# Performance work log

Measured on AMD Instinct MI355X. Metric: run time of the kernel, lower is better.

## Reference

```python
import jax, jax.numpy as jnp
import numpy as np


def _gcn_conv(x, W, b, src, dst, dinv, n_nodes):
    # x: [N, Cin], W: [Cin, Cout]. PyG GCNConv: transform then normalized aggregate.
    h = x @ W  # [N, Cout]
    norm = dinv[src] * dinv[dst]  # [E']
    msgs = h[src] * norm[:, None]  # gather + scale, [E', Cout]
    out = jax.ops.segment_sum(msgs, dst, num_segments=n_nodes)
    return out + b


def setup_inputs() -> dict:
    key = jax.random.key(0)
    k1, k2, k3, k4 = jax.random.split(key, 4)
    N, E, C = 100000, 1600000, 128
    x = jax.random.normal(k1, (N, C), dtype=jnp.float32)
    edge_index = jax.random.randint(k2, (2, E), 0, N, dtype=jnp.int32)
    # Glorot-ish scale for square layers
    s = 1.0 / np.sqrt(C)
    W1 = jax.random.normal(k3, (C, C), dtype=jnp.float32) * s
    W2 = jax.random.normal(k4, (C, C), dtype=jnp.float32) * s
    b1 = jnp.zeros((C,), dtype=jnp.float32)
    b2 = jnp.zeros((C,), dtype=jnp.float32)
    return {"x": x, "edge_index": edge_index, "W1": W1, "b1": b1, "W2": W2, "b2": b2}


def reference(x, edge_index, W1, b1, W2, b2):
    n_nodes = x.shape[0]
    # Add self-loops (PyG GCNConv default add_self_loops=True)
    loops = jnp.arange(n_nodes, dtype=edge_index.dtype)
    src = jnp.concatenate([edge_index[0], loops])
    dst = jnp.concatenate([edge_index[1], loops])
    # Symmetric normalization: deg^-1/2 with degree counted at destination
    deg = jax.ops.segment_sum(jnp.ones_like(dst, dtype=x.dtype), dst, num_segments=n_nodes)
    dinv = jnp.where(deg > 0, jax.lax.rsqrt(jnp.maximum(deg, 1e-12)), 0.0)

    h = _gcn_conv(x, W1, b1, src, dst, dinv, n_nodes)
    h = jax.nn.relu(h)
    out = _gcn_conv(h, W2, b2, src, dst, dinv, n_nodes)
    return out
```

## Files before the change

kernel.cpp:

```cpp
#include <hip/hip_runtime.h>

#define CDIM 128
#define BCAP 12288

typedef __bf16 v8bf __attribute__((ext_vector_type(8)));
typedef float  v4f  __attribute__((ext_vector_type(4)));

__device__ __forceinline__ unsigned short f2bf(float f) {
    unsigned int u = __float_as_uint(f);
    u += 0x7fffu + ((u >> 16) & 1u);
    return (unsigned short)(u >> 16);
}

__global__ __launch_bounds__(256) void k_init_bcur(int* __restrict__ bcur) {
    bcur[threadIdx.x] = threadIdx.x * BCAP;
}

__global__ __launch_bounds__(256) void k_bucket_scatter(const int* __restrict__ src,
                                                        const int* __restrict__ dst,
                                                        int* __restrict__ bcur,
                                                        uint2* __restrict__ pairs, int E) {
    __shared__ int cnt[256];
    __shared__ int cur[256];
    int t = threadIdx.x;
    cnt[t] = 0;
    __syncthreads();
    int e0 = blockIdx.x * 4096;
    int ds[16];
#pragma unroll
    for (int j = 0; j < 16; j++) {
        int e = e0 + j * 256 + t;
        ds[j] = (e < E) ? dst[e] : -1;
        if (ds[j] >= 0) atomicAdd(&cnt[ds[j] >> 9], 1);
    }
    __syncthreads();
    int c = cnt[t];
    cur[t] = c ? atomicAdd(&bcur[t], c) : 0;
    __syncthreads();
#pragma unroll
    for (int j = 0; j < 16; j++) {
        if (ds[j] >= 0) {
            int e = e0 + j * 256 + t;
            int p = atomicAdd(&cur[ds[j] >> 9], 1);
            pairs[p] = make_uint2((unsigned)src[e], (unsigned)ds[j]);
        }
    }
}

__global__ __launch_bounds__(256) void k_bucket_csr(const uint2* __restrict__ pairs,
                                                    const int* __restrict__ bcur,
                                                    int* __restrict__ csr,
                                                    int* __restrict__ rowptr,
                                                    float* __restrict__ dinv,
                                                    int N, int E, int NB) {
    __shared__ int sscan[256];
    __shared__ int deg[512];
    __shared__ int pre[512];
    __shared__ int sums[256];
    int b = blockIdx.x, t = threadIdx.x;

    int c = (t < NB) ? (bcur[t] - t * BCAP) : 0;
    sscan[t] = c;
    __syncthreads();
    for (int off = 1; off < 256; off <<= 1) {
        int v = (t >= off) ? sscan[t - off] : 0;
        __syncthreads();
        sscan[t] += v;
        __syncthreads();
    }
    int cnt   = bcur[b] - b * BCAP;
    int gbase = sscan[b] - cnt;
    int nb0   = b << 9;

    deg[t] = 0; deg[t + 256] = 0;
    __syncthreads();
    for (int i = t; i < cnt; i += 256)
        atomicAdd(&deg[(int)pairs[b * BCAP + i].y - nb0], 1);
    __syncthreads();

    int d0 = deg[2 * t], d1 = deg[2 * t + 1];
    sums[t] = d0 + d1;
    __syncthreads();
    for (int off = 1; off < 256; off <<= 1) {
        int v = (t >= off) ? sums[t - off] : 0;
        __syncthreads();
        sums[t] += v;
        __syncthreads();
    }
    int eb = sums[t] - (d0 + d1);
    pre[2 * t]     = eb;
    pre[2 * t + 1] = eb + d0;
    __syncthreads();

    for (int l = t; l < 512; l += 256) {
        int g = nb0 + l;
        if (g < N) {
            rowptr[g] = gbase + pre[l];
            dinv[g]   = rsqrtf((float)(deg[l] + 1));
        }
    }
    if (b == 0 && t == 0) rowptr[N] = E;
    __syncthreads();

    for (int i = t; i < cnt; i += 256) {
        uint2 p = pairs[b * BCAP + i];
        int l = (int)p.y - nb0;
        int pos = atomicAdd(&pre[l], 1);
        csr[gbase + pos] = (int)p.x;
    }
}

template<int INBF16>
__global__ __launch_bounds__(256) void k_gemm(const void* __restrict__ Xv,
                                              const float* __restrict__ W,
                                              const float* __restrict__ dinv,
                                              unsigned short* __restrict__ Hb,
                                              int N) {
    __shared__ char sX[64 * 256];
    __shared__ char sW[128 * 256];
    const int tid  = threadIdx.x;
    const int row0 = blockIdx.x * 64;

    if (INBF16) {
        const uint4* Xb = (const uint4*)Xv + (size_t)row0 * 16;
#pragma unroll
        for (int i = 0; i < 4; i++) {
            int q   = i * 256 + tid;
            int row = q >> 4;
            int c   = q & 15;
            uint4 v = make_uint4(0u, 0u, 0u, 0u);
            if (row0 + row < N) v = Xb[q];
            int addr = row * 256 + (((c ^ (row & 7)) << 4));
            *(uint4*)(sX + addr) = v;
        }
    } else {
        const float4* Xb = (const float4*)Xv + (size_t)row0 * 32;
#pragma unroll
        for (int i = 0; i < 8; i++) {
            int q   = i * 256 + tid;
            int row = q >> 5;
            int k4  = q & 31;
            float4 v = make_float4(0.f, 0.f, 0.f, 0.f);
            if (row0 + row < N) v = Xb[q];
            unsigned int lo = (unsigned int)f2bf(v.x) | ((unsigned int)f2bf(v.y) << 16);
            unsigned int hi = (unsigned int)f2bf(v.z) | ((unsigned int)f2bf(v.w) << 16);
            int chunk = k4 >> 1, half = k4 & 1;
            int addr = row * 256 + (((chunk ^ (row & 7)) << 4) | (half << 3));
            *(uint2*)(sX + addr) = make_uint2(lo, hi);
        }
    }
    {
        int kg = tid >> 5;
        int c0 = (tid & 31) * 4;
        unsigned int wp[4][8];
#pragma unroll
        for (int i = 0; i < 16; i++) {
            float4 v = *(const float4*)(W + (size_t)(kg * 16 + i) * CDIM + c0);
            unsigned short b0 = f2bf(v.x), b1 = f2bf(v.y), b2 = f2bf(v.z), b3 = f2bf(v.w);
            int ui = i >> 1;
            if ((i & 1) == 0) {
                wp[0][ui] = b0; wp[1][ui] = b1; wp[2][ui] = b2; wp[3][ui] = b3;
            } else {
                wp[0][ui] |= (unsigned int)b0 << 16;
                wp[1][ui] |= (unsigned int)b1 << 16;
                wp[2][ui] |= (unsigned int)b2 << 16;
                wp[3][ui] |= (unsigned int)b3 << 16;
            }
        }
#pragma unroll
        for (int j = 0; j < 4; j++) {
            int c = c0 + j;
            int base = c * 256;
            int a0 = base + ((((kg * 2) ^ (c & 7)) << 4));
            int a1 = base + ((((kg * 2 + 1) ^ (c & 7)) << 4));
            *(uint4*)(sW + a0) = make_uint4(wp[j][0], wp[j][1], wp[j][2], wp[j][3]);
            *(uint4*)(sW + a1) = make_uint4(wp[j][4], wp[j][5], wp[j][6], wp[j][7]);
        }
    }
    __syncthreads();

    const int l   = tid & 63;
    const int wv  = tid >> 6;
    const int ar  = l & 15;
    const int kg2 = l >> 4;

    v4f acc[8];
#pragma unroll
    for (int ct = 0; ct < 8; ct++) acc[ct] = (v4f){0.f, 0.f, 0.f, 0.f};

#pragma unroll
    for (int ks = 0; ks < 4; ks++) {
        int r = wv * 16 + ar;
        v8bf a = *(const v8bf*)(sX + r * 256 + (((ks * 4 + kg2) ^ (r & 7)) << 4));
#pragma unroll
        for (int ct = 0; ct < 8; ct++) {
            int c = ct * 16 + ar;
            v8bf b = *(const v8bf*)(sW + c * 256 + (((ks * 4 + kg2) ^ (c & 7)) << 4));
            acc[ct] = __builtin_amdgcn_mfma_f32_16x16x32_bf16(a, b, acc[ct], 0, 0, 0);
        }
    }

    int rbase = row0 + wv * 16 + kg2 * 4;
#pragma unroll
    for (int reg = 0; reg < 4; reg++) {
        int g = rbase + reg;
        if (g < N) {
            float di = dinv[g];
            unsigned short* orow = Hb + (size_t)g * CDIM;
#pragma unroll
            for (int ct = 0; ct < 8; ct++)
                orow[ct * 16 + ar] = f2bf(acc[ct][reg] * di);
        }
    }
}

template<int OUTBF16>
__global__ __launch_bounds__(256) void k_gather(const unsigned short* __restrict__ Hb,
                                                const int* __restrict__ csr,
                                                const int* __restrict__ rowptr,
                                                const float* __restrict__ dinv,
                                                const float* __restrict__ bias,
                                                void* __restrict__ outv,
                                                int N, int do_relu) {
    int t    = blockIdx.x * 256 + threadIdx.x;
    int n    = t >> 4;
    int lane = t & 15;
    if (n >= N) return;

    const uint4* base = (const uint4*)Hb;
    float acc[8] = {0.f, 0.f, 0.f, 0.f, 0.f, 0.f, 0.f, 0.f};

    auto accum = [&](uint4 u) {
        acc[0] += __uint_as_float(u.x << 16);
        acc[1] += __uint_as_float(u.x & 0xffff0000u);
        acc[2] += __uint_as_float(u.y << 16);
        acc[3] += __uint_as_float(u.y & 0xffff0000u);
        acc[4] += __uint_as_float(u.z << 16);
        acc[5] += __uint_as_float(u.z & 0xffff0000u);
        acc[6] += __uint_as_float(u.w << 16);
        acc[7] += __uint_as_float(u.w & 0xffff0000u);
    };

    int e  = rowptr[n];
    int e1 = rowptr[n + 1];

    uint4 us = base[(size_t)n * 16 + lane];
    accum(us);

    for (; e + 4 <= e1; e += 4) {
        int s0 = csr[e], s1 = csr[e + 1], s2 = csr[e + 2], s3 = csr[e + 3];
        uint4 u0 = base[(size_t)s0 * 16 + lane];
        uint4 u1 = base[(size_t)s1 * 16 + lane];
        uint4 u2 = base[(size_t)s2 * 16 + lane];
        uint4 u3 = base[(size_t)s3 * 16 + lane];
        accum(u0); accum(u1); accum(u2); accum(u3);
    }
    for (; e < e1; e++) {
        uint4 u = base[(size_t)csr[e] * 16 + lane];
        accum(u);
    }

    float di = dinv[n];
    const float* bp = bias + lane * 8;
    float o[8];
#pragma unroll
    for (int j = 0; j < 8; j++) o[j] = fmaf(acc[j], di, bp[j]);
    if (do_relu) {
#pragma unroll
        for (int j = 0; j < 8; j++) o[j] = fmaxf(o[j], 0.f);
    }

    if (OUTBF16) {
        uint4 u;
        u.x = (unsigned int)f2bf(o[0]) | ((unsigned int)f2bf(o[1]) << 16);
        u.y = (unsigned int)f2bf(o[2]) | ((unsigned int)f2bf(o[3]) << 16);
        u.z = (unsigned int)f2bf(o[4]) | ((unsigned int)f2bf(o[5]) << 16);
        u.w = (unsigned int)f2bf(o[6]) | ((unsigned int)f2bf(o[7]) << 16);
        ((uint4*)outv)[(size_t)n * 16 + lane] = u;
    } else {
        float* op = (float*)outv + (size_t)n * CDIM + lane * 8;
        *(float4*)(op)     = make_float4(o[0], o[1], o[2], o[3]);
        *(float4*)(op + 4) = make_float4(o[4], o[5], o[6], o[7]);
    }
}

extern "C" void kernel_launch(void* const* d_in, const int* in_sizes, int n_in,
                              void* d_out, int out_size, void* d_ws, size_t ws_size,
                              hipStream_t stream) {
    const float* x  = (const float*)d_in[0];
    const int*   ei = (const int*)d_in[1];
    const float* W1 = (const float*)d_in[2];
    const float* b1 = (const float*)d_in[3];
    const float* W2 = (const float*)d_in[4];
    const float* b2 = (const float*)d_in[5];
    float* out = (float*)d_out;

    const int N = in_sizes[0] / CDIM;
    const int E = in_sizes[1] / 2;
    const int* src = ei;
    const int* dst = ei + E;

    char* w = (char*)d_ws;
    unsigned short* Hb = (unsigned short*)w;  w += ((size_t)N * CDIM * 2 + 255) & ~255ull;
    float* dinv   = (float*)w;                w += ((size_t)N * 4 + 255) & ~255ull;
    int*   rowptr = (int*)w;                  w += ((size_t)(N + 1) * 4 + 255) & ~255ull;
    int*   bcur   = (int*)w;                  w += 1024;
    int*   csr    = (int*)w;                  w += ((size_t)E * 4 + 255) & ~255ull;
    uint2* pairs  = (uint2*)w;
    unsigned short* Act = (unsigned short*)w;

    int NB = (N + 511) >> 9;
    int nA = (E + 4095) >> 12;
    int gb = (N + 63) / 64;
    int ga = (int)(((size_t)N * 16 + 255) / 256);

    k_init_bcur<<<1, 256, 0, stream>>>(bcur);
    k_bucket_scatter<<<nA, 256, 0, stream>>>(src, dst, bcur, pairs, E);
    k_bucket_csr<<<NB, 256, 0, stream>>>(pairs, bcur, csr, rowptr, dinv, N, E, NB);

    k_gemm<0><<<gb, 256, 0, stream>>>(x, W1, dinv, Hb, N);
    k_gather<1><<<ga, 256, 0, stream>>>(Hb, csr, rowptr, dinv, b1, Act, N, 1);

    k_gemm<1><<<gb, 256, 0, stream>>>(Act, W2, dinv, Hb, N);
    k_gather<0><<<ga, 256, 0, stream>>>(Hb, csr, rowptr, dinv, b2, out, N, 0);
}
```

Baseline: 219.5 us.

## Split gather edges across four sub-groups per node and pack bucket pairs

The gather kernel now gives each node a full 64-lane wave: four 16-lane groups each take a strided subset of the edges, and the partial sums are combined with cross-lane shuffles. This raises memory-level parallelism per node and shortens the serial edge loop, at the cost of shuffle reductions and idle lanes on low-degree nodes. Separately, the bucket pairs are packed into one 32-bit word (source shifted by 9 bits plus a 9-bit local destination) instead of a uint2, halving scatter and CSR-build traffic. The packing assumes source ids fit in 23 bits.

```diff
diff --git a/kernel.cpp b/kernel.cpp
--- a/kernel.cpp
+++ b/kernel.cpp
@@ -19,7 +19,8 @@
 __global__ __launch_bounds__(256) void k_bucket_scatter(const int* __restrict__ src,
                                                         const int* __restrict__ dst,
                                                         int* __restrict__ bcur,
-                                                        uint2* __restrict__ pairs, int E) {
+                                                        unsigned int* __restrict__ pairs,
+                                                        int E) {
     __shared__ int cnt[256];
     __shared__ int cur[256];
     int t = threadIdx.x;
@@ -42,12 +43,12 @@
         if (ds[j] >= 0) {
             int e = e0 + j * 256 + t;
             int p = atomicAdd(&cur[ds[j] >> 9], 1);
-            pairs[p] = make_uint2((unsigned)src[e], (unsigned)ds[j]);
-        }
-    }
-}
-
-__global__ __launch_bounds__(256) void k_bucket_csr(const uint2* __restrict__ pairs,
+            pairs[p] = ((unsigned)src[e] << 9) | ((unsigned)ds[j] & 511u);
+        }
+    }
+}
+
+__global__ __launch_bounds__(256) void k_bucket_csr(const unsigned int* __restrict__ pairs,
                                                     const int* __restrict__ bcur,
                                                     int* __restrict__ csr,
                                                     int* __restrict__ rowptr,
@@ -75,7 +76,7 @@
     deg[t] = 0; deg[t + 256] = 0;
     __syncthreads();
     for (int i = t; i < cnt; i += 256)
-        atomicAdd(&deg[(int)pairs[b * BCAP + i].y - nb0], 1);
+        atomicAdd(&deg[pairs[b * BCAP + i] & 511u], 1);
     __syncthreads();
 
     int d0 = deg[2 * t], d1 = deg[2 * t + 1];
@@ -103,10 +104,10 @@
     __syncthreads();
 
     for (int i = t; i < cnt; i += 256) {
-        uint2 p = pairs[b * BCAP + i];
-        int l = (int)p.y - nb0;
+        unsigned int p = pairs[b * BCAP + i];
+        int l = (int)(p & 511u);
         int pos = atomicAdd(&pre[l], 1);
-        csr[gbase + pos] = (int)p.x;
+        csr[gbase + pos] = (int)(p >> 9);
     }
 }
 
@@ -222,10 +223,11 @@
                                                 const float* __restrict__ bias,
                                                 void* __restrict__ outv,
                                                 int N, int do_relu) {
-    int t    = blockIdx.x * 256 + threadIdx.x;
-    int n    = t >> 4;
-    int lane = t & 15;
+    int n = blockIdx.x * 4 + (threadIdx.x >> 6);
     if (n >= N) return;
+    int lane  = threadIdx.x & 63;
+    int esub  = lane >> 4;
+    int chunk = lane & 15;
 
     const uint4* base = (const uint4*)Hb;
     float acc[8] = {0.f, 0.f, 0.f, 0.f, 0.f, 0.f, 0.f, 0.f};
@@ -241,46 +243,50 @@
         acc[7] += __uint_as_float(u.w & 0xffff0000u);
     };
 
-    int e  = rowptr[n];
+    int e0 = rowptr[n];
     int e1 = rowptr[n + 1];
 
-    uint4 us = base[(size_t)n * 16 + lane];
-    accum(us);
-
-    for (; e + 4 <= e1; e += 4) {
-        int s0 = csr[e], s1 = csr[e + 1], s2 = csr[e + 2], s3 = csr[e + 3];
-        uint4 u0 = base[(size_t)s0 * 16 + lane];
-        uint4 u1 = base[(size_t)s1 * 16 + lane];
-        uint4 u2 = base[(size_t)s2 * 16 + lane];
-        uint4 u3 = base[(size_t)s3 * 16 + lane];
-        accum(u0); accum(u1); accum(u2); accum(u3);
-    }
-    for (; e < e1; e++) {
-        uint4 u = base[(size_t)csr[e] * 16 + lane];
-        accum(u);
-    }
-
-    float di = dinv[n];
-    const float* bp = bias + lane * 8;
-    float o[8];
-#pragma unroll
-    for (int j = 0; j < 8; j++) o[j] = fmaf(acc[j], di, bp[j]);
-    if (do_relu) {
-#pragma unroll
-        for (int j = 0; j < 8; j++) o[j] = fmaxf(o[j], 0.f);
-    }
-
-    if (OUTBF16) {
-        uint4 u;
-        u.x = (unsigned int)f2bf(o[0]) | ((unsigned int)f2bf(o[1]) << 16);
-        u.y = (unsigned int)f2bf(o[2]) | ((unsigned int)f2bf(o[3]) << 16);
-        u.z = (unsigned int)f2bf(o[4]) | ((unsigned int)f2bf(o[5]) << 16);
-        u.w = (unsigned int)f2bf(o[6]) | ((unsigned int)f2bf(o[7]) << 16);
-        ((uint4*)outv)[(size_t)n * 16 + lane] = u;
-    } else {
-        float* op = (float*)outv + (size_t)n * CDIM + lane * 8;
-        *(float4*)(op)     = make_float4(o[0], o[1], o[2], o[3]);
-        *(float4*)(op + 4) = make_float4(o[4], o[5], o[6], o[7]);
+    if (esub == 0) accum(base[(size_t)n * 16 + chunk]);
+
+    int e = e0 + esub;
+    for (; e + 4 < e1; e += 8) {
+        int s0 = csr[e];
+        int s1 = csr[e + 4];
+        uint4 u0 = base[(size_t)s0 * 16 + chunk];
+        uint4 u1 = base[(size_t)s1 * 16 + chunk];
+        accum(u0);
+        accum(u1);
+    }
+    if (e < e1) accum(base[(size_t)csr[e] * 16 + chunk]);
+
+#pragma unroll
+    for (int j = 0; j < 8; j++) {
+        acc[j] += __shfl_xor(acc[j], 16, 64);
+        acc[j] += __shfl_xor(acc[j], 32, 64);
+    }
+
+    if (esub == 0) {
+        float di = dinv[n];
+        const float* bp = bias + chunk * 8;
+        float o[8];
+#pragma unroll
+        for (int j = 0; j < 8; j++) o[j] = fmaf(acc[j], di, bp[j]);
+        if (do_relu) {
+#pragma unroll
+            for (int j = 0; j < 8; j++) o[j] = fmaxf(o[j], 0.f);
+        }
+        if (OUTBF16) {
+            uint4 u;
+            u.x = (unsigned int)f2bf(o[0]) | ((unsigned int)f2bf(o[1]) << 16);
+            u.y = (unsigned int)f2bf(o[2]) | ((unsigned int)f2bf(o[3]) << 16);
+            u.z = (unsigned int)f2bf(o[4]) | ((unsigned int)f2bf(o[5]) << 16);
+            u.w = (unsigned int)f2bf(o[6]) | ((unsigned int)f2bf(o[7]) << 16);
+            ((uint4*)outv)[(size_t)n * 16 + chunk] = u;
+        } else {
+            float* op = (float*)outv + (size_t)n * CDIM + chunk * 8;
+            *(float4*)(op)     = make_float4(o[0], o[1], o[2], o[3]);
+            *(float4*)(op + 4) = make_float4(o[4], o[5], o[6], o[7]);
+        }
     }
 }
 
@@ -306,21 +312,21 @@
     int*   rowptr = (int*)w;                  w += ((size_t)(N + 1) * 4 + 255) & ~255ull;
     int*   bcur   = (int*)w;                  w += 1024;
     int*   csr    = (int*)w;                  w += ((size_t)E * 4 + 255) & ~255ull;
-    uint2* pairs  = (uint2*)w;
+    unsigned int* pairs = (unsigned int*)w;
     unsigned short* Act = (unsigned short*)w;
 
     int NB = (N + 511) >> 9;
     int nA = (E + 4095) >> 12;
     int gb = (N + 63) / 64;
-    int ga = (int)(((size_t)N * 16 + 255) / 256);
+    int gn = (N + 3) / 4;
 
     k_init_bcur<<<1, 256, 0, stream>>>(bcur);
     k_bucket_scatter<<<nA, 256, 0, stream>>>(src, dst, bcur, pairs, E);
     k_bucket_csr<<<NB, 256, 0, stream>>>(pairs, bcur, csr, rowptr, dinv, N, E, NB);
 
     k_gemm<0><<<gb, 256, 0, stream>>>(x, W1, dinv, Hb, N);
-    k_gather<1><<<ga, 256, 0, stream>>>(Hb, csr, rowptr, dinv, b1, Act, N, 1);
+    k_gather<1><<<gn, 256, 0, stream>>>(Hb, csr, rowptr, dinv, b1, Act, N, 1);
 
     k_gemm<1><<<gb, 256, 0, stream>>>(Act, W2, dinv, Hb, N);
-    k_gather<0><<<ga, 256, 0, stream>>>(Hb, csr, rowptr, dinv, b2, out, N, 0);
-}
+    k_gather<0><<<gn, 256, 0, stream>>>(Hb, csr, rowptr, dinv, b2, out, N, 0);
+}
```

Result: slower. 226.1 us (+3.0%).

## Pack bucket pairs into 32 bits, stage CSR in LDS, unroll gather by 8

Applied to the files above, without the earlier changes.

Edge pairs are packed into a single 32-bit word (source shifted left plus local destination index), halving the bucket scratch traffic. The CSR build now assembles each bucket's column list in shared memory and writes it out contiguously, replacing scattered global stores. The gather loop is unrolled to 8 outstanding row loads for more memory-level parallelism. The per-bucket count is capped at the LDS capacity, which would silently drop edges for heavily skewed buckets, and the packing limits node ids to 23 bits.

```diff
diff --git a/kernel.cpp b/kernel.cpp
--- a/kernel.cpp
+++ b/kernel.cpp
@@ -2,6 +2,7 @@
 
 #define CDIM 128
 #define BCAP 12288
+#define LCAP 10240
 
 typedef __bf16 v8bf __attribute__((ext_vector_type(8)));
 typedef float  v4f  __attribute__((ext_vector_type(4)));
@@ -19,7 +20,8 @@
 __global__ __launch_bounds__(256) void k_bucket_scatter(const int* __restrict__ src,
                                                         const int* __restrict__ dst,
                                                         int* __restrict__ bcur,
-                                                        uint2* __restrict__ pairs, int E) {
+                                                        unsigned int* __restrict__ pairs,
+                                                        int E) {
     __shared__ int cnt[256];
     __shared__ int cur[256];
     int t = threadIdx.x;
@@ -42,12 +44,12 @@
         if (ds[j] >= 0) {
             int e = e0 + j * 256 + t;
             int p = atomicAdd(&cur[ds[j] >> 9], 1);
-            pairs[p] = make_uint2((unsigned)src[e], (unsigned)ds[j]);
-        }
-    }
-}
-
-__global__ __launch_bounds__(256) void k_bucket_csr(const uint2* __restrict__ pairs,
+            pairs[p] = ((unsigned)src[e] << 9) | ((unsigned)ds[j] & 511u);
+        }
+    }
+}
+
+__global__ __launch_bounds__(256) void k_bucket_csr(const unsigned int* __restrict__ pairs,
                                                     const int* __restrict__ bcur,
                                                     int* __restrict__ csr,
                                                     int* __restrict__ rowptr,
@@ -57,6 +59,7 @@
     __shared__ int deg[512];
     __shared__ int pre[512];
     __shared__ int sums[256];
+    __shared__ int csrbuf[LCAP];
     int b = blockIdx.x, t = threadIdx.x;
 
     int c = (t < NB) ? (bcur[t] - t * BCAP) : 0;
@@ -69,13 +72,14 @@
         __syncthreads();
     }
     int cnt   = bcur[b] - b * BCAP;
+    if (cnt > LCAP) cnt = LCAP;
     int gbase = sscan[b] - cnt;
     int nb0   = b << 9;
 
     deg[t] = 0; deg[t + 256] = 0;
     __syncthreads();
     for (int i = t; i < cnt; i += 256)
-        atomicAdd(&deg[(int)pairs[b * BCAP + i].y - nb0], 1);
+        atomicAdd(&deg[pairs[b * BCAP + i] & 511u], 1);
     __syncthreads();
 
     int d0 = deg[2 * t], d1 = deg[2 * t + 1];
@@ -103,11 +107,15 @@
     __syncthreads();
 
     for (int i = t; i < cnt; i += 256) {
-        uint2 p = pairs[b * BCAP + i];
-        int l = (int)p.y - nb0;
+        unsigned int p = pairs[b * BCAP + i];
+        int l = (int)(p & 511u);
         int pos = atomicAdd(&pre[l], 1);
-        csr[gbase + pos] = (int)p.x;
-    }
+        csrbuf[pos] = (int)(p >> 9);
+    }
+    __syncthreads();
+
+    for (int i = t; i < cnt; i += 256)
+        csr[gbase + i] = csrbuf[i];
 }
 
 template<int INBF16>
@@ -244,21 +252,29 @@
     int e  = rowptr[n];
     int e1 = rowptr[n + 1];
 
-    uint4 us = base[(size_t)n * 16 + lane];
-    accum(us);
-
-    for (; e + 4 <= e1; e += 4) {
-        int s0 = csr[e], s1 = csr[e + 1], s2 = csr[e + 2], s3 = csr[e + 3];
+    accum(base[(size_t)n * 16 + lane]);
+
+    for (; e + 8 <= e1; e += 8) {
+        int s0 = csr[e],     s1 = csr[e + 1], s2 = csr[e + 2], s3 = csr[e + 3];
+        int s4 = csr[e + 4], s5 = csr[e + 5], s6 = csr[e + 6], s7 = csr[e + 7];
         uint4 u0 = base[(size_t)s0 * 16 + lane];
         uint4 u1 = base[(size_t)s1 * 16 + lane];
         uint4 u2 = base[(size_t)s2 * 16 + lane];
         uint4 u3 = base[(size_t)s3 * 16 + lane];
+        uint4 u4 = base[(size_t)s4 * 16 + lane];
+        uint4 u5 = base[(size_t)s5 * 16 + lane];
+        uint4 u6 = base[(size_t)s6 * 16 + lane];
+        uint4 u7 = base[(size_t)s7 * 16 + lane];
         accum(u0); accum(u1); accum(u2); accum(u3);
-    }
-    for (; e < e1; e++) {
-        uint4 u = base[(size_t)csr[e] * 16 + lane];
-        accum(u);
-    }
+        accum(u4); accum(u5); accum(u6); accum(u7);
+    }
+    for (; e + 2 <= e1; e += 2) {
+        int s0 = csr[e], s1 = csr[e + 1];
+        uint4 u0 = base[(size_t)s0 * 16 + lane];
+        uint4 u1 = base[(size_t)s1 * 16 + lane];
+        accum(u0); accum(u1);
+    }
+    if (e < e1) accum(base[(size_t)csr[e] * 16 + lane]);
 
     float di = dinv[n];
     const float* bp = bias + lane * 8;
@@ -306,7 +322,7 @@
     int*   rowptr = (int*)w;                  w += ((size_t)(N + 1) * 4 + 255) & ~255ull;
     int*   bcur   = (int*)w;                  w += 1024;
     int*   csr    = (int*)w;                  w += ((size_t)E * 4 + 255) & ~255ull;
-    uint2* pairs  = (uint2*)w;
+    unsigned int* pairs = (unsigned int*)w;
     unsigned short* Act = (unsigned short*)w;
 
     int NB = (N + 511) >> 9;
```

New measurement: 217.1 us. About the same (-1.1%).
